# Kernel tuning notes

Hardware: AMD Instinct MI355X
Metric: run time of the kernel (lower is better)

Reference implementation:

```python
import jax, jax.numpy as jnp
import numpy as np

EMBED_DIM = 400          # d; entity embedding is 2d (alpha|beta)
N_ENTITY = 100000
N_RELATION = 500
HIDDEN = 1600
BATCH = 8192


def _reg(x):
    # Regularizer(base_add=1, min_val=0.05, max_val=1e9)
    return jnp.clip(x + 1.0, 0.05, 1e9)


def setup_inputs() -> dict:
    key = jax.random.key(0)
    ks = jax.random.split(key, 16)
    d = EMBED_DIM
    rng = (9.0 + 2.0) / d  # (gamma + epsilon) / embed_dim with gamma=9

    def xavier(k, shape):
        fan_out, fan_in = shape
        lim = np.sqrt(6.0 / (fan_in + fan_out))
        return jax.random.uniform(k, shape, jnp.float32, -lim, lim)

    inp = {
        "anchor1_idx": jax.random.randint(ks[0], (BATCH,), 0, N_ENTITY),
        "rel1_idx": jax.random.randint(ks[1], (BATCH,), 0, N_RELATION),
        "anchor2_idx": jax.random.randint(ks[2], (BATCH,), 0, N_ENTITY),
        "rel2_idx": jax.random.randint(ks[3], (BATCH,), 0, N_RELATION),
        # embedding tables
        "entity_embedding": jax.random.uniform(ks[4], (N_ENTITY, 2 * d), jnp.float32, -rng, rng),
        "relation_embedding": jax.random.uniform(ks[5], (N_RELATION, d), jnp.float32, -rng, rng),
        # BetaProjection: layer1 [hidden, 2d+d], layer2 [hidden, hidden], layer0 [2d, hidden]
        "pW1": xavier(ks[6], (HIDDEN, 3 * d)),
        "pb1": jnp.zeros((HIDDEN,), jnp.float32),
        "pW2": xavier(ks[7], (HIDDEN, HIDDEN)),
        "pb2": jnp.zeros((HIDDEN,), jnp.float32),
        "pW0": xavier(ks[8], (2 * d, HIDDEN)),
        "pb0": jnp.zeros((2 * d,), jnp.float32),
        # BetaIntersection: layer1 [2d, 2d], layer2 [d, 2d]
        "iW1": xavier(ks[9], (2 * d, 2 * d)),
        "ib1": jnp.zeros((2 * d,), jnp.float32),
        "iW2": xavier(ks[10], (d, 2 * d)),
        "ib2": jnp.zeros((d,), jnp.float32),
    }
    return inp


def _projection(e_emb, r_emb, pW1, pb1, pW2, pb2, pW0, pb0):
    # cat -> Linear+ReLU (layer1) -> Linear+ReLU (layer2) -> layer0 -> regularizer
    x = jnp.concatenate([e_emb, r_emb], axis=-1)           # [B, 3d]
    x = jax.nn.relu(x @ pW1.T + pb1)                       # [B, H]
    x = jax.nn.relu(x @ pW2.T + pb2)                       # [B, H]
    x = x @ pW0.T + pb0                                    # [B, 2d]
    return _reg(x)


def _intersection(alphas, betas, iW1, ib1, iW2, ib2):
    # alphas/betas: [K, B, d]; softmax attention over K
    all_emb = jnp.concatenate([alphas, betas], axis=-1)    # [K, B, 2d]
    h = jax.nn.relu(all_emb @ iW1.T + ib1)                 # [K, B, 2d]
    att = jax.nn.softmax(h @ iW2.T + ib2, axis=0)          # [K, B, d]
    return jnp.sum(att * alphas, axis=0), jnp.sum(att * betas, axis=0)


def reference(anchor1_idx, rel1_idx, anchor2_idx, rel2_idx,
              entity_embedding, relation_embedding,
              pW1, pb1, pW2, pb2, pW0, pb0,
              iW1, ib1, iW2, ib2):
    h = _reg(entity_embedding)                             # entity_regularizer
    r = relation_embedding

    emb1 = _projection(h[anchor1_idx], r[rel1_idx], pW1, pb1, pW2, pb2, pW0, pb0)
    a1, b1 = jnp.split(emb1, 2, axis=-1)
    emb2 = _projection(h[anchor2_idx], r[rel2_idx], pW1, pb1, pW2, pb2, pW0, pb0)
    a2, b2 = jnp.split(emb2, 2, axis=-1)

    alpha, beta = _intersection(jnp.stack([a1, a2]), jnp.stack([b1, b2]),
                                iW1, ib1, iW2, ib2)
    return alpha, beta
```

## Files before the change

kernel.cpp:

```cpp
#include <hip/hip_runtime.h>
#include <hip/hip_bf16.h>
#include <stdint.h>

typedef __bf16 bf16_t;
typedef __bf16 bf16x8 __attribute__((ext_vector_type(8)));
typedef float f32x4 __attribute__((ext_vector_type(4)));

constexpr int BATCH = 8192;
constexpr int M = 2 * BATCH;

constexpr int K1 = 1216;
constexpr int N1c = 1792, N1s = 1664;
constexpr int K2 = 1664;
constexpr int N2c = 1792, N2s = 1664;
constexpr int K3 = 1664;
constexpr int N3c = 1024, N3s = 1024;
constexpr int K4 = 1024;
constexpr int N4c = 1024, N4s = 1024;
constexpr int K5 = 1024, N5 = 512;

__device__ __forceinline__ void gload_lds16(const void* g, void* l) {
  __builtin_amdgcn_global_load_lds(
      (const __attribute__((address_space(1))) void*)g,
      (__attribute__((address_space(3))) void*)l,
      16, 0, 0);
}

#define CFENCE() asm volatile("" ::: "memory")
#define BAR()  { CFENCE(); __builtin_amdgcn_s_barrier(); CFENCE(); }

__global__ void gather_kernel(const int* __restrict__ a1, const int* __restrict__ r1,
                              const int* __restrict__ a2, const int* __restrict__ r2,
                              const float* __restrict__ ent, const float* __restrict__ rel,
                              bf16_t* __restrict__ X) {
  const int row = blockIdx.x;
  const int b   = row & (BATCH - 1);
  const int br  = row >> 13;
  const int eidx = br ? a2[b] : a1[b];
  const int ridx = br ? r2[b] : r1[b];
  const float* __restrict__ esrc = ent + (size_t)eidx * 800;
  const float* __restrict__ rsrc = rel + (size_t)ridx * 400;
  bf16_t* __restrict__ dst = X + (size_t)row * K1;

  for (int g = threadIdx.x; g < K1 / 4; g += 256) {
    const int c = g * 4;
    float4 v = make_float4(0.f, 0.f, 0.f, 0.f);
    if (c < 800) {
      v = *(const float4*)(esrc + c);
      v.x = fminf(fmaxf(v.x + 1.f, 0.05f), 1e9f);
      v.y = fminf(fmaxf(v.y + 1.f, 0.05f), 1e9f);
      v.z = fminf(fmaxf(v.z + 1.f, 0.05f), 1e9f);
      v.w = fminf(fmaxf(v.w + 1.f, 0.05f), 1e9f);
    } else if (c < 1200) {
      v = *(const float4*)(rsrc + (c - 800));
    }
    union { bf16_t h[4]; uint2 u; } pk;
    pk.h[0] = (bf16_t)v.x; pk.h[1] = (bf16_t)v.y;
    pk.h[2] = (bf16_t)v.z; pk.h[3] = (bf16_t)v.w;
    *(uint2*)(dst + c) = pk.u;
  }
}

__global__ void convw_kernel(const float* __restrict__ src, bf16_t* __restrict__ dst,
                             int Nr, int Kc, int Kp, int total4) {
  const int idx = blockIdx.x * 256 + threadIdx.x;
  if (idx >= total4) return;
  const int kp4 = Kp >> 2;
  const int r = idx / kp4;
  const int c = (idx - r * kp4) << 2;
  union { bf16_t h[4]; uint2 u; } pk;
#pragma unroll
  for (int j = 0; j < 4; ++j) {
    const int cc = c + j;
    const float v = (r < Nr && cc < Kc) ? src[(size_t)r * Kc + cc] : 0.f;
    pk.h[j] = (bf16_t)v;
  }
  *(uint2*)(dst + (size_t)r * Kp + c) = pk.u;
}

enum { ACT_RELU = 0, ACT_REG = 1, ACT_NONE = 2 };

template <int ACT, int OUTMODE>
__global__ __launch_bounds__(512)
void gemm256(const bf16_t* __restrict__ A, const bf16_t* __restrict__ Bw,
             const float* __restrict__ bias, int Nbias,
             bf16_t* __restrict__ Cb, float* __restrict__ Cf,
             int Kd, int Nstore, int NT, int gridN) {
  __shared__ __align__(16) bf16_t lds[8][8192];

  const int nwg = gridDim.x;
  const int id = blockIdx.x;
  const int swz = (id & 7) * (nwg >> 3) + (id >> 3);
  const int bn = swz % gridN, bm = swz / gridN;

  const int t = threadIdx.x;
  const int lane = t & 63;
  const int wv = t >> 6;
  const int wm = wv >> 2, wn = wv & 3;
  const int l15 = lane & 15;
  const int kbs = ((lane >> 4) << 4) ^ ((lane & 3) << 4);

  const int srow = t >> 2;
  const int skc  = (t & 3) ^ (srow & 3);
  const bf16_t* aR0 = A  + (size_t)(bm * 256 + srow) * Kd + skc * 8;
  const bf16_t* aR1 = aR0 + (size_t)128 * Kd;
  const bf16_t* bR0 = Bw + (size_t)(bn * 256 + srow) * Kd + skc * 8;
  const bf16_t* bR1 = bR0 + (size_t)128 * Kd;
  const int ldsb0 = (wv * 64) * 16;
  const int ldsb1 = (512 + wv * 64) * 16;

  auto STAGE = [&](const bf16_t* r0p, const bf16_t* r1p, int kOff, bf16_t* slot) {
    gload_lds16(r0p + kOff, (char*)slot + ldsb0);
    gload_lds16(r1p + kOff, (char*)slot + ldsb1);
  };

  f32x4 acc[8][4];
#pragma unroll
  for (int i = 0; i < 8; ++i)
#pragma unroll
    for (int j = 0; j < 4; ++j) acc[i][j] = f32x4{0.f, 0.f, 0.f, 0.f};

  STAGE(aR0, aR1, 0, lds[0]);
  STAGE(bR0, bR1, 0, lds[2]);
  STAGE(aR0, aR1, 32, lds[1]);
  STAGE(bR0, bR1, 32, lds[3]);
  if (NT > 1) {
    STAGE(aR0, aR1, 64, lds[4]);
    STAGE(bR0, bR1, 64, lds[6]);
    asm volatile("s_waitcnt vmcnt(8)" ::: "memory");
  } else {
    asm volatile("s_waitcnt vmcnt(4)" ::: "memory");
  }
  __builtin_amdgcn_s_barrier();
  CFENCE();

  bf16x8 bfr[4];
  int db = 0;
  for (int kt = 0; kt < NT; ++kt, db ^= 1) {
    const bool p1 = (kt + 1) < NT;
    const bool p2 = (kt + 2) < NT;
    bf16_t* const cur = (bf16_t*)lds[db * 4];
    bf16_t* const nxt = (bf16_t*)lds[(db ^ 1) * 4];

    {
      const char* sA = (const char*)(cur);
      const char* sB = (const char*)(cur + 2 * 8192);
      bf16x8 af[4];
#pragma unroll
      for (int i = 0; i < 4; ++i)
        af[i] = *(const bf16x8*)(sA + ((wm * 128 + i * 16 + l15) << 6) + kbs);
#pragma unroll
      for (int i = 0; i < 4; ++i)
        bfr[i] = *(const bf16x8*)(sB + ((wn * 64 + i * 16 + l15) << 6) + kbs);
      if (p1) STAGE(aR0, aR1, (kt + 1) * 64 + 32, nxt + 1 * 8192);
      BAR();
      __builtin_amdgcn_s_setprio(1);
#pragma unroll
      for (int i = 0; i < 4; ++i)
#pragma unroll
        for (int j = 0; j < 4; ++j)
          acc[i][j] = __builtin_amdgcn_mfma_f32_16x16x32_bf16(af[i], bfr[j], acc[i][j], 0, 0, 0);
      __builtin_amdgcn_s_setprio(0);
      BAR();
    }
    {
      const char* sA = (const char*)(cur);
      bf16x8 af[4];
#pragma unroll
      for (int i = 0; i < 4; ++i)
        af[i] = *(const bf16x8*)(sA + ((wm * 128 + (4 + i) * 16 + l15) << 6) + kbs);
      if (p1) STAGE(bR0, bR1, (kt + 1) * 64 + 32, nxt + 3 * 8192);
      BAR();
      __builtin_amdgcn_s_setprio(1);
#pragma unroll
      for (int i = 0; i < 4; ++i)
#pragma unroll
        for (int j = 0; j < 4; ++j)
          acc[4 + i][j] = __builtin_amdgcn_mfma_f32_16x16x32_bf16(af[i], bfr[j], acc[4 + i][j], 0, 0, 0);
      __builtin_amdgcn_s_setprio(0);
      if (p1) asm volatile("s_waitcnt vmcnt(8)" ::: "memory");
      else    asm volatile("s_waitcnt vmcnt(0)" ::: "memory");
      BAR();
    }
    {
      const char* sA = (const char*)(cur + 1 * 8192);
      const char* sB = (const char*)(cur + 3 * 8192);
      bf16x8 af[4];
#pragma unroll
      for (int i = 0; i < 4; ++i)
        af[i] = *(const bf16x8*)(sA + ((wm * 128 + i * 16 + l15) << 6) + kbs);
#pragma unroll
      for (int i = 0; i < 4; ++i)
        bfr[i] = *(const bf16x8*)(sB + ((wn * 64 + i * 16 + l15) << 6) + kbs);
      if (p2) STAGE(aR0, aR1, (kt + 2) * 64, cur + 0 * 8192);
      BAR();
      __builtin_amdgcn_s_setprio(1);
#pragma unroll
      for (int i = 0; i < 4; ++i)
#pragma unroll
        for (int j = 0; j < 4; ++j)
          acc[i][j] = __builtin_amdgcn_mfma_f32_16x16x32_bf16(af[i], bfr[j], acc[i][j], 0, 0, 0);
      __builtin_amdgcn_s_setprio(0);
      BAR();
    }
    {
      const char* sA = (const char*)(cur + 1 * 8192);
      bf16x8 af[4];
#pragma unroll
      for (int i = 0; i < 4; ++i)
        af[i] = *(const bf16x8*)(sA + ((wm * 128 + (4 + i) * 16 + l15) << 6) + kbs);
      if (p2) STAGE(bR0, bR1, (kt + 2) * 64, cur + 2 * 8192);
      BAR();
      __builtin_amdgcn_s_setprio(1);
#pragma unroll
      for (int i = 0; i < 4; ++i)
#pragma unroll
        for (int j = 0; j < 4; ++j)
          acc[4 + i][j] = __builtin_amdgcn_mfma_f32_16x16x32_bf16(af[i], bfr[j], acc[4 + i][j], 0, 0, 0);
      __builtin_amdgcn_s_setprio(0);
      if (p1) {
        if (p2) asm volatile("s_waitcnt vmcnt(8)" ::: "memory");
        else    asm volatile("s_waitcnt vmcnt(4)" ::: "memory");
      }
      BAR();
    }
  }

  const int r0 = bm * 256 + wm * 128 + ((lane >> 4) * 4);
  const int c0 = bn * 256 + wn * 64 + l15;
#pragma unroll
  for (int ni = 0; ni < 4; ++ni) {
    const int col = c0 + ni * 16;
    const float bv = (col < Nbias) ? bias[col] : 0.f;
    const bool cok = (col < Nstore);
#pragma unroll
    for (int mi = 0; mi < 8; ++mi) {
#pragma unroll
      for (int j = 0; j < 4; ++j) {
        float v = acc[mi][ni][j] + bv;
        if (ACT == ACT_RELU) v = fmaxf(v, 0.f);
        else if (ACT == ACT_REG) v = fminf(fmaxf(v + 1.f, 0.05f), 1e9f);
        if (cok) {
          const size_t off = (size_t)(r0 + mi * 16 + j) * Nstore + col;
          if (OUTMODE == 0 || OUTMODE == 2) Cb[off] = (bf16_t)v;
          if (OUTMODE == 1 || OUTMODE == 2) Cf[off] = v;
        }
      }
    }
  }
}

template <int ACT, int OUTMODE>
__global__ __launch_bounds__(256)
void gemm_kernel(const bf16_t* __restrict__ A, const bf16_t* __restrict__ Bw,
                 const float* __restrict__ bias, int Nbias,
                 bf16_t* __restrict__ Cb, float* __restrict__ Cf,
                 int Kd, int Nd) {
  __shared__ __align__(16) bf16_t As[128 * 64];
  __shared__ __align__(16) bf16_t Bs[128 * 64];

  const int bn = blockIdx.x, bm = blockIdx.y;
  const int t = threadIdx.x;
  const int lane = t & 63;
  const int wv = t >> 6;
  const int wm = wv >> 1, wn = wv & 1;

  f32x4 acc[4][4];
#pragma unroll
  for (int i = 0; i < 4; ++i)
#pragma unroll
    for (int j = 0; j < 4; ++j) acc[i][j] = f32x4{0.f, 0.f, 0.f, 0.f};

  const size_t aBase = (size_t)(bm * 128) * Kd;
  const size_t bBase = (size_t)(bn * 128) * Kd;

  for (int kt = 0; kt < Kd; kt += 64) {
    __syncthreads();
#pragma unroll
    for (int q = 0; q < 4; ++q) {
      const int lin = q * 256 + t;
      const int row = lin >> 3;
      const int kc = (lin & 7) * 8;
      const int lofs = (q * 256 + wv * 64) * 16;
      gload_lds16(A + aBase + (size_t)row * Kd + kt + kc, (char*)As + lofs);
      gload_lds16(Bw + bBase + (size_t)row * Kd + kt + kc, (char*)Bs + lofs);
    }
    __syncthreads();

#pragma unroll
    for (int s = 0; s < 2; ++s) {
      const int k0 = s * 32 + ((lane >> 4) * 8);
      bf16x8 af[4], bf[4];
#pragma unroll
      for (int i = 0; i < 4; ++i) {
        const int ra = wm * 64 + i * 16 + (lane & 15);
        af[i] = *(const bf16x8*)(As + ra * 64 + k0);
        const int rb = wn * 64 + i * 16 + (lane & 15);
        bf[i] = *(const bf16x8*)(Bs + rb * 64 + k0);
      }
#pragma unroll
      for (int mi = 0; mi < 4; ++mi)
#pragma unroll
        for (int ni = 0; ni < 4; ++ni)
          acc[mi][ni] = __builtin_amdgcn_mfma_f32_16x16x32_bf16(af[mi], bf[ni], acc[mi][ni], 0, 0, 0);
    }
  }

  const int r0 = bm * 128 + wm * 64 + ((lane >> 4) * 4);
  const int c0 = bn * 128 + wn * 64 + (lane & 15);
#pragma unroll
  for (int ni = 0; ni < 4; ++ni) {
    const int col = c0 + ni * 16;
    const float bv = (col < Nbias) ? bias[col] : 0.f;
#pragma unroll
    for (int mi = 0; mi < 4; ++mi) {
#pragma unroll
      for (int j = 0; j < 4; ++j) {
        float v = acc[mi][ni][j] + bv;
        if (ACT == ACT_RELU) v = fmaxf(v, 0.f);
        else if (ACT == ACT_REG) v = fminf(fmaxf(v + 1.f, 0.05f), 1e9f);
        const size_t off = (size_t)(r0 + mi * 16 + j) * Nd + col;
        if (OUTMODE == 0 || OUTMODE == 2) Cb[off] = (bf16_t)v;
        if (OUTMODE == 1 || OUTMODE == 2) Cf[off] = v;
      }
    }
  }
}

__global__ void combine_kernel(const float* __restrict__ L, const float* __restrict__ E,
                               float* __restrict__ out) {
  const int i = blockIdx.x * 256 + threadIdx.x;
  const int b = i / 400;
  const int d = i - b * 400;
  const float l1 = L[(size_t)b * N5 + d];
  const float l2 = L[(size_t)(BATCH + b) * N5 + d];
  const float att1 = 1.f / (1.f + expf(l2 - l1));
  const float att2 = 1.f - att1;
  const float* E1 = E + (size_t)b * N3s;
  const float* E2 = E + (size_t)(BATCH + b) * N3s;
  out[i] = att1 * E1[d] + att2 * E2[d];
  out[(size_t)BATCH * 400 + i] = att1 * E1[400 + d] + att2 * E2[400 + d];
}

extern "C" void kernel_launch(void* const* d_in, const int* in_sizes, int n_in,
                              void* d_out, int out_size, void* d_ws, size_t ws_size,
                              hipStream_t stream) {
  const int* a1 = (const int*)d_in[0];
  const int* r1 = (const int*)d_in[1];
  const int* a2 = (const int*)d_in[2];
  const int* r2 = (const int*)d_in[3];
  const float* ent = (const float*)d_in[4];
  const float* rel = (const float*)d_in[5];
  const float* pW1 = (const float*)d_in[6];
  const float* pb1 = (const float*)d_in[7];
  const float* pW2 = (const float*)d_in[8];
  const float* pb2 = (const float*)d_in[9];
  const float* pW0 = (const float*)d_in[10];
  const float* pb0 = (const float*)d_in[11];
  const float* iW1 = (const float*)d_in[12];
  const float* ib1 = (const float*)d_in[13];
  const float* iW2 = (const float*)d_in[14];
  const float* ib2 = (const float*)d_in[15];

  char* ws = (char*)d_ws;
  size_t o = 0;
  auto take = [&](size_t bytes) { char* p = ws + o; o += (bytes + 255) & ~(size_t)255; return p; };
  bf16_t* W1b  = (bf16_t*)take((size_t)N1c * K1 * 2);
  bf16_t* W2b  = (bf16_t*)take((size_t)N2c * K2 * 2);
  bf16_t* W0b  = (bf16_t*)take((size_t)N3c * K3 * 2);
  bf16_t* iW1b = (bf16_t*)take((size_t)N4c * K4 * 2);
  bf16_t* iW2b = (bf16_t*)take((size_t)N5 * K5 * 2);
  char* bufX = take((size_t)M * K1 * 2);
  char* bufY = take((size_t)M * N1s * 2);
  char* bufZ = take((size_t)M * N2s * 2);
  float* Ef  = (float*)take((size_t)M * N3s * 4);

  bf16_t* Xb = (bf16_t*)bufX;
  bf16_t* Yb = (bf16_t*)bufY;
  bf16_t* Zb = (bf16_t*)bufZ;
  bf16_t* Eb = (bf16_t*)bufX;
  bf16_t* Hb = (bf16_t*)bufY;
  float*  Lf = (float*)bufZ;

  auto cgrid = [](int n4) { return dim3((n4 + 255) / 256); };
  convw_kernel<<<cgrid(N1c * K1 / 4), 256, 0, stream>>>(pW1, W1b, 1600, 1200, K1, N1c * K1 / 4);
  convw_kernel<<<cgrid(N2c * K2 / 4), 256, 0, stream>>>(pW2, W2b, 1600, 1600, K2, N2c * K2 / 4);
  convw_kernel<<<cgrid(N3c * K3 / 4), 256, 0, stream>>>(pW0, W0b, 800, 1600, K3, N3c * K3 / 4);
  convw_kernel<<<cgrid(N4c * K4 / 4), 256, 0, stream>>>(iW1, iW1b, 800, 800, K4, N4c * K4 / 4);
  convw_kernel<<<cgrid(N5 * K5 / 4), 256, 0, stream>>>(iW2, iW2b, 400, 800, K5, N5 * K5 / 4);

  gather_kernel<<<M, 256, 0, stream>>>(a1, r1, a2, r2, ent, rel, Xb);

  gemm256<ACT_RELU, 0><<<dim3((N1c / 256) * (M / 256)), 512, 0, stream>>>(
      Xb, W1b, pb1, 1600, Yb, nullptr, K1, N1s, K1 / 64, N1c / 256);
  gemm256<ACT_RELU, 0><<<dim3((N2c / 256) * (M / 256)), 512, 0, stream>>>(
      Yb, W2b, pb2, 1600, Zb, nullptr, K2, N2s, K2 / 64, N2c / 256);
  gemm256<ACT_REG, 2><<<dim3((N3c / 256) * (M / 256)), 512, 0, stream>>>(
      Zb, W0b, pb0, 800, Eb, Ef, K3, N3s, K3 / 64, N3c / 256);
  gemm256<ACT_RELU, 0><<<dim3((N4c / 256) * (M / 256)), 512, 0, stream>>>(
      Eb, iW1b, ib1, 800, Hb, nullptr, K4, N4s, K4 / 64, N4c / 256);
  gemm_kernel<ACT_NONE, 1><<<dim3(N5 / 128, M / 128), 256, 0, stream>>>(
      Hb, iW2b, ib2, 400, nullptr, Lf, K5, N5);

  combine_kernel<<<(BATCH * 400) / 256, 256, 0, stream>>>(Lf, Ef, (float*)d_out);
}
```

Measured before the change: 418.7 us.

## Trim padded K loops, change LDS swizzles, and merge weight conversions

Decouples the leading dimension from the K loop length so the GEMMs stop iterating over zero-padded K columns (1664→1600, 1024→832). The LDS XOR swizzle is changed in both GEMM kernels to reduce bank conflicts on fragment reads. The five weight-conversion launches are merged into one kernel. Risk: 1600/64 = 25 tiles, an odd count, may interact badly with the double-buffered pipeline in gemm256, and the swizzle must match on the write and read sides.

```diff
diff --git a/kernel.cpp b/kernel.cpp
--- a/kernel.cpp
+++ b/kernel.cpp
@@ -11,13 +11,13 @@
 
 constexpr int K1 = 1216;
 constexpr int N1c = 1792, N1s = 1664;
-constexpr int K2 = 1664;
+constexpr int LDA2 = 1664, KL2 = 1600;
 constexpr int N2c = 1792, N2s = 1664;
-constexpr int K3 = 1664;
+constexpr int LDA3 = 1664, KL3 = 1600;
 constexpr int N3c = 1024, N3s = 1024;
-constexpr int K4 = 1024;
+constexpr int LDA4 = 1024, KL4 = 832;
 constexpr int N4c = 1024, N4s = 1024;
-constexpr int K5 = 1024, N5 = 512;
+constexpr int LDA5 = 1024, KL5 = 832, N5 = 512;
 
 __device__ __forceinline__ void gload_lds16(const void* g, void* l) {
   __builtin_amdgcn_global_load_lds(
@@ -61,10 +61,8 @@
   }
 }
 
-__global__ void convw_kernel(const float* __restrict__ src, bf16_t* __restrict__ dst,
-                             int Nr, int Kc, int Kp, int total4) {
-  const int idx = blockIdx.x * 256 + threadIdx.x;
-  if (idx >= total4) return;
+__device__ __forceinline__ void doconv(int idx, const float* __restrict__ src,
+                                       bf16_t* __restrict__ dst, int Nr, int Kc, int Kp) {
   const int kp4 = Kp >> 2;
   const int r = idx / kp4;
   const int c = (idx - r * kp4) << 2;
@@ -76,6 +74,26 @@
     pk.h[j] = (bf16_t)v;
   }
   *(uint2*)(dst + (size_t)r * Kp + c) = pk.u;
+}
+
+constexpr int CJ0 = N1c * K1 / 4;
+constexpr int CJ1 = CJ0 + N2c * LDA2 / 4;
+constexpr int CJ2 = CJ1 + N3c * LDA3 / 4;
+constexpr int CJ3 = CJ2 + N4c * LDA4 / 4;
+constexpr int CJ4 = CJ3 + N5 * LDA5 / 4;
+
+__global__ void convw5_kernel(const float* __restrict__ pW1, const float* __restrict__ pW2,
+                              const float* __restrict__ pW0, const float* __restrict__ iW1,
+                              const float* __restrict__ iW2,
+                              bf16_t* __restrict__ W1b, bf16_t* __restrict__ W2b,
+                              bf16_t* __restrict__ W0b, bf16_t* __restrict__ iW1b,
+                              bf16_t* __restrict__ iW2b) {
+  int idx = blockIdx.x * 256 + threadIdx.x;
+  if (idx < CJ0)      doconv(idx,        pW1, W1b, 1600, 1200, K1);
+  else if (idx < CJ1) doconv(idx - CJ0,  pW2, W2b, 1600, 1600, LDA2);
+  else if (idx < CJ2) doconv(idx - CJ1,  pW0, W0b,  800, 1600, LDA3);
+  else if (idx < CJ3) doconv(idx - CJ2,  iW1, iW1b, 800,  800, LDA4);
+  else                doconv(idx - CJ3,  iW2, iW2b, 400,  800, LDA5);
 }
 
 enum { ACT_RELU = 0, ACT_REG = 1, ACT_NONE = 2 };
@@ -85,7 +103,7 @@
 void gemm256(const bf16_t* __restrict__ A, const bf16_t* __restrict__ Bw,
              const float* __restrict__ bias, int Nbias,
              bf16_t* __restrict__ Cb, float* __restrict__ Cf,
-             int Kd, int Nstore, int NT, int gridN) {
+             int lda, int Nstore, int NT, int gridN) {
   __shared__ __align__(16) bf16_t lds[8][8192];
 
   const int nwg = gridDim.x;
@@ -98,14 +116,14 @@
   const int wv = t >> 6;
   const int wm = wv >> 2, wn = wv & 3;
   const int l15 = lane & 15;
-  const int kbs = ((lane >> 4) << 4) ^ ((lane & 3) << 4);
+  const int kbs = (((lane >> 4) ^ ((l15 >> 1) & 3)) << 4);
 
   const int srow = t >> 2;
-  const int skc  = (t & 3) ^ (srow & 3);
-  const bf16_t* aR0 = A  + (size_t)(bm * 256 + srow) * Kd + skc * 8;
-  const bf16_t* aR1 = aR0 + (size_t)128 * Kd;
-  const bf16_t* bR0 = Bw + (size_t)(bn * 256 + srow) * Kd + skc * 8;
-  const bf16_t* bR1 = bR0 + (size_t)128 * Kd;
+  const int skc  = (t & 3) ^ ((t >> 3) & 3);
+  const bf16_t* aR0 = A  + (size_t)(bm * 256 + srow) * lda + skc * 8;
+  const bf16_t* aR1 = aR0 + (size_t)128 * lda;
+  const bf16_t* bR0 = Bw + (size_t)(bn * 256 + srow) * lda + skc * 8;
+  const bf16_t* bR1 = bR0 + (size_t)128 * lda;
   const int ldsb0 = (wv * 64) * 16;
   const int ldsb1 = (512 + wv * 64) * 16;
 
@@ -255,7 +273,7 @@
 void gemm_kernel(const bf16_t* __restrict__ A, const bf16_t* __restrict__ Bw,
                  const float* __restrict__ bias, int Nbias,
                  bf16_t* __restrict__ Cb, float* __restrict__ Cf,
-                 int Kd, int Nd) {
+                 int lda, int Kloop, int Nd) {
   __shared__ __align__(16) bf16_t As[128 * 64];
   __shared__ __align__(16) bf16_t Bs[128 * 64];
 
@@ -271,25 +289,26 @@
 #pragma unroll
     for (int j = 0; j < 4; ++j) acc[i][j] = f32x4{0.f, 0.f, 0.f, 0.f};
 
-  const size_t aBase = (size_t)(bm * 128) * Kd;
-  const size_t bBase = (size_t)(bn * 128) * Kd;
-
-  for (int kt = 0; kt < Kd; kt += 64) {
+  const size_t aBase = (size_t)(bm * 128) * lda;
+  const size_t bBase = (size_t)(bn * 128) * lda;
+
+  for (int kt = 0; kt < Kloop; kt += 64) {
     __syncthreads();
 #pragma unroll
     for (int q = 0; q < 4; ++q) {
       const int lin = q * 256 + t;
       const int row = lin >> 3;
-      const int kc = (lin & 7) * 8;
+      const int kc = ((lin & 7) ^ ((lin >> 3) & 7)) * 8;
       const int lofs = (q * 256 + wv * 64) * 16;
-      gload_lds16(A + aBase + (size_t)row * Kd + kt + kc, (char*)As + lofs);
-      gload_lds16(Bw + bBase + (size_t)row * Kd + kt + kc, (char*)Bs + lofs);
+      gload_lds16(A + aBase + (size_t)row * lda + kt + kc, (char*)As + lofs);
+      gload_lds16(Bw + bBase + (size_t)row * lda + kt + kc, (char*)Bs + lofs);
     }
     __syncthreads();
 
 #pragma unroll
     for (int s = 0; s < 2; ++s) {
-      const int k0 = s * 32 + ((lane >> 4) * 8);
+      const int crd = s * 4 + (lane >> 4);
+      const int k0 = (crd ^ (lane & 7)) * 8;
       bf16x8 af[4], bf[4];
 #pragma unroll
       for (int i = 0; i < 4; ++i) {
@@ -366,10 +385,10 @@
   size_t o = 0;
   auto take = [&](size_t bytes) { char* p = ws + o; o += (bytes + 255) & ~(size_t)255; return p; };
   bf16_t* W1b  = (bf16_t*)take((size_t)N1c * K1 * 2);
-  bf16_t* W2b  = (bf16_t*)take((size_t)N2c * K2 * 2);
-  bf16_t* W0b  = (bf16_t*)take((size_t)N3c * K3 * 2);
-  bf16_t* iW1b = (bf16_t*)take((size_t)N4c * K4 * 2);
-  bf16_t* iW2b = (bf16_t*)take((size_t)N5 * K5 * 2);
+  bf16_t* W2b  = (bf16_t*)take((size_t)N2c * LDA2 * 2);
+  bf16_t* W0b  = (bf16_t*)take((size_t)N3c * LDA3 * 2);
+  bf16_t* iW1b = (bf16_t*)take((size_t)N4c * LDA4 * 2);
+  bf16_t* iW2b = (bf16_t*)take((size_t)N5 * LDA5 * 2);
   char* bufX = take((size_t)M * K1 * 2);
   char* bufY = take((size_t)M * N1s * 2);
   char* bufZ = take((size_t)M * N2s * 2);
@@ -382,25 +401,21 @@
   bf16_t* Hb = (bf16_t*)bufY;
   float*  Lf = (float*)bufZ;
 
-  auto cgrid = [](int n4) { return dim3((n4 + 255) / 256); };
-  convw_kernel<<<cgrid(N1c * K1 / 4), 256, 0, stream>>>(pW1, W1b, 1600, 1200, K1, N1c * K1 / 4);
-  convw_kernel<<<cgrid(N2c * K2 / 4), 256, 0, stream>>>(pW2, W2b, 1600, 1600, K2, N2c * K2 / 4);
-  convw_kernel<<<cgrid(N3c * K3 / 4), 256, 0, stream>>>(pW0, W0b, 800, 1600, K3, N3c * K3 / 4);
-  convw_kernel<<<cgrid(N4c * K4 / 4), 256, 0, stream>>>(iW1, iW1b, 800, 800, K4, N4c * K4 / 4);
-  convw_kernel<<<cgrid(N5 * K5 / 4), 256, 0, stream>>>(iW2, iW2b, 400, 800, K5, N5 * K5 / 4);
+  convw5_kernel<<<dim3(CJ4 / 256), 256, 0, stream>>>(pW1, pW2, pW0, iW1, iW2,
+                                                     W1b, W2b, W0b, iW1b, iW2b);
 
   gather_kernel<<<M, 256, 0, stream>>>(a1, r1, a2, r2, ent, rel, Xb);
 
   gemm256<ACT_RELU, 0><<<dim3((N1c / 256) * (M / 256)), 512, 0, stream>>>(
       Xb, W1b, pb1, 1600, Yb, nullptr, K1, N1s, K1 / 64, N1c / 256);
   gemm256<ACT_RELU, 0><<<dim3((N2c / 256) * (M / 256)), 512, 0, stream>>>(
-      Yb, W2b, pb2, 1600, Zb, nullptr, K2, N2s, K2 / 64, N2c / 256);
+      Yb, W2b, pb2, 1600, Zb, nullptr, LDA2, N2s, KL2 / 64, N2c / 256);
   gemm256<ACT_REG, 2><<<dim3((N3c / 256) * (M / 256)), 512, 0, stream>>>(
-      Zb, W0b, pb0, 800, Eb, Ef, K3, N3s, K3 / 64, N3c / 256);
+      Zb, W0b, pb0, 800, Eb, Ef, LDA3, N3s, KL3 / 64, N3c / 256);
   gemm256<ACT_RELU, 0><<<dim3((N4c / 256) * (M / 256)), 512, 0, stream>>>(
-      Eb, iW1b, ib1, 800, Hb, nullptr, K4, N4s, K4 / 64, N4c / 256);
+      Eb, iW1b, ib1, 800, Hb, nullptr, LDA4, N4s, KL4 / 64, N4c / 256);
   gemm_kernel<ACT_NONE, 1><<<dim3(N5 / 128, M / 128), 256, 0, stream>>>(
-      Hb, iW2b, ib2, 400, nullptr, Lf, K5, N5);
+      Hb, iW2b, ib2, 400, nullptr, Lf, LDA5, KL5, N5);
 
   combine_kernel<<<(BATCH * 400) / 256, 256, 0, stream>>>(Lf, Ef, (float*)d_out);
 }
```

Result: faster. 367.8 us (-12.1%).
